# Kernel optimization log

Hardware: AMD Instinct MI355X
Metric: run time of the kernel (lower is better)

The kernel has to match this reference:

```python
import jax, jax.numpy as jnp
import numpy as np

N = 40000      # nodes
E = 640000     # edges
G = 64         # graphs in batch
F_IN = 128
H = 128


def setup_inputs() -> dict:
    key = jax.random.key(0)
    ks = jax.random.split(key, 10)
    x = jax.random.normal(ks[0], (N, F_IN), dtype=jnp.float32)
    edge_index = jax.random.randint(ks[1], (2, E), 0, N, dtype=jnp.int64)
    batch = jnp.sort(jax.random.randint(ks[2], (N,), 0, G, dtype=jnp.int64))
    s = 0.05
    W1 = jax.random.normal(ks[3], (F_IN, H), dtype=jnp.float32) * s
    W2 = jax.random.normal(ks[4], (H, H), dtype=jnp.float32) * s
    W3 = jax.random.normal(ks[5], (H, H), dtype=jnp.float32) * s
    Wl = jax.random.normal(ks[6], (H, 1), dtype=jnp.float32) * s
    b1 = jnp.zeros((H,), jnp.float32)
    b2 = jnp.zeros((H,), jnp.float32)
    b3 = jnp.zeros((H,), jnp.float32)
    bl = jnp.zeros((1,), jnp.float32)
    return {"x": x, "edge_index": edge_index, "batch": batch, "dropout_rate": 0,
            "W1": W1, "b1": b1, "W2": W2, "b2": b2, "W3": W3, "b3": b3,
            "Wl": Wl, "bl": bl}


def _gcn_norm(edge_index, n):
    # PyG GCNConv default: add self-loops, symmetric deg^{-1/2} normalization.
    loop = jnp.arange(n, dtype=edge_index.dtype)
    row = jnp.concatenate([edge_index[0], loop])  # source
    col = jnp.concatenate([edge_index[1], loop])  # target
    ones = jnp.ones(row.shape[0], jnp.float32)
    deg = jax.ops.segment_sum(ones, col, num_segments=n)
    dis = jnp.where(deg > 0, jax.lax.rsqrt(deg), 0.0)
    norm = dis[row] * dis[col]  # [E+N]
    return row, col, norm


def _gcn_conv(x, row, col, norm, W, b, n):
    h = x @ W + b                       # dense transform [N,H]
    msg = h[row] * norm[:, None]        # gather + scale  [E+N,H]
    return jax.ops.segment_sum(msg, col, num_segments=n)


def reference(x, edge_index, batch, dropout_rate, W1, b1, W2, b2, W3, b3, Wl, bl):
    n = x.shape[0]
    row, col, norm = _gcn_norm(edge_index, n)
    # eval mode: dropout(p=dropout_rate, training=False) is identity
    h = jax.nn.relu(_gcn_conv(x, row, col, norm, W1, b1, n))
    h = jax.nn.relu(_gcn_conv(h, row, col, norm, W2, b2, n))
    h = jax.nn.relu(_gcn_conv(h, row, col, norm, W3, b3, n))
    # global mean pool over graphs
    sums = jax.ops.segment_sum(h, batch, num_segments=G)           # [G,H]
    cnt = jax.ops.segment_sum(jnp.ones(n, jnp.float32), batch, num_segments=G)
    pooled = sums / jnp.maximum(cnt, 1.0)[:, None]
    return pooled @ Wl + bl             # [G,1]
```

## Files before the change

### kernel.cpp

```cpp
#include <hip/hip_runtime.h>

constexpr int N = 40000;
constexpr int E = 640000;
constexpr int G = 64;
constexpr int H = 128;

constexpr int NB      = (N + 255) / 256;
constexpr int EB      = (E + 255) / 256;
constexpr int GEMM_B  = N / 32;
constexpr int FUSED_B = N / 32;
constexpr int CSR_MAX = E + 8 * N;

typedef float floatx2 __attribute__((ext_vector_type(2)));

__device__ __forceinline__ unsigned pack_fp8x4(float a, float b, float c, float d) {
    unsigned v = 0;
    v = __builtin_amdgcn_cvt_pk_fp8_f32(a, b, v, false);
    v = __builtin_amdgcn_cvt_pk_fp8_f32(c, d, v, true);
    return v;
}

__device__ __forceinline__ void fma8(float4& acc, unsigned r, float w) {
    floatx2 lo = __builtin_amdgcn_cvt_pk_f32_fp8(r, false);
    floatx2 hi = __builtin_amdgcn_cvt_pk_f32_fp8(r, true);
    acc.x = fmaf(lo.x, w, acc.x);
    acc.y = fmaf(lo.y, w, acc.y);
    acc.z = fmaf(hi.x, w, acc.z);
    acc.w = fmaf(hi.y, w, acc.w);
}

__device__ __forceinline__ float entry_w(int e) {
    floatx2 hi = __builtin_amdgcn_cvt_pk_f32_fp8((unsigned)e, true);
    return hi.y;
}
__device__ __forceinline__ int entry_src(int e) { return e & 0xFFFFFF; }

__device__ __forceinline__ float4 aggregate_node(const unsigned* __restrict__ h8,
                                                 const int4* __restrict__ csr4,
                                                 const int* __restrict__ row_ptr,
                                                 const float* __restrict__ dis,
                                                 int i, int c) {
    float d = dis[i];
    float sl = d * d;
    float4 acc = make_float4(0.f, 0.f, 0.f, 0.f);
    fma8(acc, h8[(size_t)i * 32 + c], sl);
    int p  = row_ptr[i] >> 2;
    int p1 = row_ptr[i + 1] >> 2;
    for (; p < p1; p += 2) {
        int4 ea = csr4[p], eb = csr4[p + 1];
        unsigned r0 = h8[(size_t)entry_src(ea.x) * 32 + c];
        unsigned r1 = h8[(size_t)entry_src(ea.y) * 32 + c];
        unsigned r2 = h8[(size_t)entry_src(ea.z) * 32 + c];
        unsigned r3 = h8[(size_t)entry_src(ea.w) * 32 + c];
        unsigned r4 = h8[(size_t)entry_src(eb.x) * 32 + c];
        unsigned r5 = h8[(size_t)entry_src(eb.y) * 32 + c];
        unsigned r6 = h8[(size_t)entry_src(eb.z) * 32 + c];
        unsigned r7 = h8[(size_t)entry_src(eb.w) * 32 + c];
        fma8(acc, r0, entry_w(ea.x)); fma8(acc, r1, entry_w(ea.y));
        fma8(acc, r2, entry_w(ea.z)); fma8(acc, r3, entry_w(ea.w));
        fma8(acc, r4, entry_w(eb.x)); fma8(acc, r5, entry_w(eb.y));
        fma8(acc, r6, entry_w(eb.z)); fma8(acc, r7, entry_w(eb.w));
    }
    return acc;
}

__global__ __launch_bounds__(256) void gemm1_and_count(const float* __restrict__ X,
                                                       const float* __restrict__ W,
                                                       const float* __restrict__ b,
                                                       unsigned* __restrict__ Y,
                                                       const int* __restrict__ col,
                                                       int* __restrict__ deg) {
    __shared__ float4 Ws4[64 * 32];
    const int blk = blockIdx.x;
    const int tid = threadIdx.x;
    if (blk >= GEMM_B) {
        int e = (blk - GEMM_B) * 256 + tid;
        if (e < E) atomicAdd(&deg[col[e]], 1);
        return;
    }
    const int jg = tid & 31;
    const int rs = tid >> 5;
    const int r0 = blk * 32 + rs * 4;

    const float4* W4 = reinterpret_cast<const float4*>(W);
    const float4* X4 = reinterpret_cast<const float4*>(X);

    const float4 bv = reinterpret_cast<const float4*>(b)[jg];
    float4 acc0 = bv, acc1 = bv, acc2 = bv, acc3 = bv;

    for (int half = 0; half < 2; ++half) {
        #pragma unroll
        for (int i = 0; i < 8; ++i)
            Ws4[tid + i * 256] = W4[half * 2048 + tid + i * 256];
        __syncthreads();

        #pragma unroll 4
        for (int k4 = 0; k4 < 16; ++k4) {
            float4 xv0 = X4[(size_t)(r0 + 0) * 32 + half * 16 + k4];
            float4 xv1 = X4[(size_t)(r0 + 1) * 32 + half * 16 + k4];
            float4 xv2 = X4[(size_t)(r0 + 2) * 32 + half * 16 + k4];
            float4 xv3 = X4[(size_t)(r0 + 3) * 32 + half * 16 + k4];
            #pragma unroll
            for (int kk = 0; kk < 4; ++kk) {
                float4 wv = Ws4[(k4 * 4 + kk) * 32 + jg];
                float xs0 = (kk==0)?xv0.x:(kk==1)?xv0.y:(kk==2)?xv0.z:xv0.w;
                float xs1 = (kk==0)?xv1.x:(kk==1)?xv1.y:(kk==2)?xv1.z:xv1.w;
                float xs2 = (kk==0)?xv2.x:(kk==1)?xv2.y:(kk==2)?xv2.z:xv2.w;
                float xs3 = (kk==0)?xv3.x:(kk==1)?xv3.y:(kk==2)?xv3.z:xv3.w;
                acc0.x = fmaf(xs0, wv.x, acc0.x); acc0.y = fmaf(xs0, wv.y, acc0.y);
                acc0.z = fmaf(xs0, wv.z, acc0.z); acc0.w = fmaf(xs0, wv.w, acc0.w);
                acc1.x = fmaf(xs1, wv.x, acc1.x); acc1.y = fmaf(xs1, wv.y, acc1.y);
                acc1.z = fmaf(xs1, wv.z, acc1.z); acc1.w = fmaf(xs1, wv.w, acc1.w);
                acc2.x = fmaf(xs2, wv.x, acc2.x); acc2.y = fmaf(xs2, wv.y, acc2.y);
                acc2.z = fmaf(xs2, wv.z, acc2.z); acc2.w = fmaf(xs2, wv.w, acc2.w);
                acc3.x = fmaf(xs3, wv.x, acc3.x); acc3.y = fmaf(xs3, wv.y, acc3.y);
                acc3.z = fmaf(xs3, wv.z, acc3.z); acc3.w = fmaf(xs3, wv.w, acc3.w);
            }
        }
        __syncthreads();
    }

    Y[(size_t)(r0 + 0) * 32 + jg] = pack_fp8x4(acc0.x, acc0.y, acc0.z, acc0.w);
    Y[(size_t)(r0 + 1) * 32 + jg] = pack_fp8x4(acc1.x, acc1.y, acc1.z, acc1.w);
    Y[(size_t)(r0 + 2) * 32 + jg] = pack_fp8x4(acc2.x, acc2.y, acc2.z, acc2.w);
    Y[(size_t)(r0 + 3) * 32 + jg] = pack_fp8x4(acc3.x, acc3.y, acc3.z, acc3.w);
}

__global__ void dis_block_sum(const int* __restrict__ deg, float* __restrict__ dis,
                              int* __restrict__ part) {
    __shared__ int s[256];
    int i = blockIdx.x * 256 + threadIdx.x;
    int d = (i < N) ? deg[i] : 0;
    if (i < N) dis[i] = rsqrtf((float)(d + 1));
    s[threadIdx.x] = (d + 7) & ~7;
    __syncthreads();
    for (int off = 128; off > 0; off >>= 1) {
        if (threadIdx.x < off) s[threadIdx.x] += s[threadIdx.x + off];
        __syncthreads();
    }
    if (threadIdx.x == 0) part[blockIdx.x] = s[0];
}

__global__ void scan_write(const int* __restrict__ deg, const int* __restrict__ part,
                           int* __restrict__ row_ptr, int* __restrict__ cursor) {
    __shared__ int s[256];
    const int t = threadIdx.x;
    s[t] = (t < (int)blockIdx.x) ? part[t] : 0;
    __syncthreads();
    for (int o = 128; o > 0; o >>= 1) {
        if (t < o) s[t] += s[t + o];
        __syncthreads();
    }
    const int block_off = s[0];
    __syncthreads();
    int i = blockIdx.x * 256 + t;
    int val = (i < N) ? ((deg[i] + 7) & ~7) : 0;
    s[t] = val;
    __syncthreads();
    for (int o = 1; o < 256; o <<= 1) {
        int x = (t >= o) ? s[t - o] : 0;
        __syncthreads();
        s[t] += x;
        __syncthreads();
    }
    if (i < N) {
        int excl = s[t] - val + block_off;
        row_ptr[i] = excl;
        cursor[i] = excl;
        if (i == N - 1) row_ptr[N] = excl + val;
    }
}

__global__ void fill_csr(const int* __restrict__ row, const int* __restrict__ col,
                         const float* __restrict__ dis, int* __restrict__ cursor,
                         int* __restrict__ csr) {
    int e = blockIdx.x * blockDim.x + threadIdx.x;
    if (e >= E) return;
    int r = row[e], c = col[e];
    float w = dis[r] * dis[c];
    unsigned wb = __builtin_amdgcn_cvt_pk_fp8_f32(w, 0.0f, 0, false) & 0xFFu;
    int p = atomicAdd(&cursor[c], 1);
    csr[p] = (int)((wb << 24) | (unsigned)r);
}

__global__ __launch_bounds__(256) void fused_agg_gemm(const unsigned* __restrict__ t_in,
                                                      const int4* __restrict__ csr4,
                                                      const int* __restrict__ row_ptr,
                                                      const float* __restrict__ dis,
                                                      const float* __restrict__ W,
                                                      const float* __restrict__ b,
                                                      unsigned* __restrict__ t_out) {
    __shared__ float4 tile[32 * 32];
    const int tid = threadIdx.x;
    const int node0 = blockIdx.x * 32;

    {
        const int c  = tid & 31;
        const int nl = tid >> 5;
        #pragma unroll
        for (int sub = 0; sub < 4; ++sub) {
            const int local = sub * 8 + nl;
            float4 acc = aggregate_node(t_in, csr4, row_ptr, dis, node0 + local, c);
            acc.x = fmaxf(acc.x, 0.f); acc.y = fmaxf(acc.y, 0.f);
            acc.z = fmaxf(acc.z, 0.f); acc.w = fmaxf(acc.w, 0.f);
            tile[local * 32 + c] = acc;
        }
    }
    __syncthreads();

    const int jg = tid & 31;
    const int rs = tid >> 5;
    const int r0 = rs * 4;
    const float4* W4 = reinterpret_cast<const float4*>(W);
    const float4 bv = reinterpret_cast<const float4*>(b)[jg];
    float4 acc0 = bv, acc1 = bv, acc2 = bv, acc3 = bv;

    #pragma unroll 4
    for (int k4 = 0; k4 < 32; ++k4) {
        float4 xv0 = tile[(r0 + 0) * 32 + k4];
        float4 xv1 = tile[(r0 + 1) * 32 + k4];
        float4 xv2 = tile[(r0 + 2) * 32 + k4];
        float4 xv3 = tile[(r0 + 3) * 32 + k4];
        #pragma unroll
        for (int kk = 0; kk < 4; ++kk) {
            float4 wv = W4[(k4 * 4 + kk) * 32 + jg];
            float xs0 = (kk==0)?xv0.x:(kk==1)?xv0.y:(kk==2)?xv0.z:xv0.w;
            float xs1 = (kk==0)?xv1.x:(kk==1)?xv1.y:(kk==2)?xv1.z:xv1.w;
            float xs2 = (kk==0)?xv2.x:(kk==1)?xv2.y:(kk==2)?xv2.z:xv2.w;
            float xs3 = (kk==0)?xv3.x:(kk==1)?xv3.y:(kk==2)?xv3.z:xv3.w;
            acc0.x = fmaf(xs0, wv.x, acc0.x); acc0.y = fmaf(xs0, wv.y, acc0.y);
            acc0.z = fmaf(xs0, wv.z, acc0.z); acc0.w = fmaf(xs0, wv.w, acc0.w);
            acc1.x = fmaf(xs1, wv.x, acc1.x); acc1.y = fmaf(xs1, wv.y, acc1.y);
            acc1.z = fmaf(xs1, wv.z, acc1.z); acc1.w = fmaf(xs1, wv.w, acc1.w);
            acc2.x = fmaf(xs2, wv.x, acc2.x); acc2.y = fmaf(xs2, wv.y, acc2.y);
            acc2.z = fmaf(xs2, wv.z, acc2.z); acc2.w = fmaf(xs2, wv.w, acc2.w);
            acc3.x = fmaf(xs3, wv.x, acc3.x); acc3.y = fmaf(xs3, wv.y, acc3.y);
            acc3.z = fmaf(xs3, wv.z, acc3.z); acc3.w = fmaf(xs3, wv.w, acc3.w);
        }
    }

    const int gr0 = node0 + r0;
    t_out[(size_t)(gr0 + 0) * 32 + jg] = pack_fp8x4(acc0.x, acc0.y, acc0.z, acc0.w);
    t_out[(size_t)(gr0 + 1) * 32 + jg] = pack_fp8x4(acc1.x, acc1.y, acc1.z, acc1.w);
    t_out[(size_t)(gr0 + 2) * 32 + jg] = pack_fp8x4(acc2.x, acc2.y, acc2.z, acc2.w);
    t_out[(size_t)(gr0 + 3) * 32 + jg] = pack_fp8x4(acc3.x, acc3.y, acc3.z, acc3.w);
}

__global__ __launch_bounds__(256) void agg_pool(const unsigned* __restrict__ t_in,
                                                const int4* __restrict__ csr4,
                                                const int* __restrict__ row_ptr,
                                                const float* __restrict__ dis,
                                                const int* __restrict__ batch,
                                                float* __restrict__ pooled) {
    __shared__ float4 tile[8 * 32];
    const int tid = threadIdx.x;
    const int c  = tid & 31;
    const int nl = tid >> 5;
    const int i0 = blockIdx.x * 8;

    float4 acc = aggregate_node(t_in, csr4, row_ptr, dis, i0 + nl, c);
    acc.x = fmaxf(acc.x, 0.f); acc.y = fmaxf(acc.y, 0.f);
    acc.z = fmaxf(acc.z, 0.f); acc.w = fmaxf(acc.w, 0.f);
    tile[nl * 32 + c] = acc;
    __syncthreads();

    if (tid < 128) {
        const int j = tid;
        const float* tf = reinterpret_cast<const float*>(tile);
        int cur = batch[i0];
        float s = 0.0f;
        #pragma unroll
        for (int r = 0; r < 8; ++r) {
            int g = batch[i0 + r];
            if (g != cur) { atomicAdd(&pooled[cur * H + j], s); s = 0.0f; cur = g; }
            s += tf[r * 128 + j];
        }
        atomicAdd(&pooled[cur * H + j], s);
    }
}

__global__ __launch_bounds__(128) void head(const float* __restrict__ pooled,
                                            const int* __restrict__ batch,
                                            const float* __restrict__ Wl,
                                            const float* __restrict__ bl,
                                            float* __restrict__ out) {
    const int g = blockIdx.x;
    const int j = threadIdx.x;
    __shared__ int bounds[2];
    if (j < 2) {
        int target = g + j;
        int lo = 0, hi = N;
        while (lo < hi) {
            int mid = (lo + hi) >> 1;
            if (batch[mid] < target) lo = mid + 1; else hi = mid;
        }
        bounds[j] = lo;
    }
    __syncthreads();
    float cnt = fmaxf((float)(bounds[1] - bounds[0]), 1.0f);
    float val = (pooled[g * H + j] / cnt) * Wl[j];
    __shared__ float red[128];
    red[j] = val;
    __syncthreads();
    #pragma unroll
    for (int s = 64; s > 0; s >>= 1) {
        if (j < s) red[j] += red[j + s];
        __syncthreads();
    }
    if (j == 0) out[g] = red[0] + bl[0];
}

extern "C" void kernel_launch(void* const* d_in, const int* in_sizes, int n_in,
                              void* d_out, int out_size, void* d_ws, size_t ws_size,
                              hipStream_t stream) {
    const float* x     = (const float*)d_in[0];
    const int*   ei    = (const int*)  d_in[1];
    const int*   batch = (const int*)  d_in[2];
    const float* W1 = (const float*)d_in[4];
    const float* b1 = (const float*)d_in[5];
    const float* W2 = (const float*)d_in[6];
    const float* b2 = (const float*)d_in[7];
    const float* W3 = (const float*)d_in[8];
    const float* b3 = (const float*)d_in[9];
    const float* Wl = (const float*)d_in[10];
    const float* bl = (const float*)d_in[11];
    float* out = (float*)d_out;

    const int* row = ei;
    const int* col = ei + E;

    auto align256 = [](size_t v) { return (v + 255) & ~(size_t)255; };
    char* ws = (char*)d_ws;
    size_t off = 0;
    int*   deg    = (int*)(ws + off);
    float* pooled = (float*)(deg + N);
    int*   csr    = (int*)(pooled + (size_t)G * H);
    size_t zero_bytes = (size_t)N * 4 + (size_t)G * H * 4 + (size_t)CSR_MAX * 4;
    off += align256(zero_bytes);
    float*    dis     = (float*)(ws + off); off += align256((size_t)N * 4);
    int*      row_ptr = (int*)  (ws + off); off += align256((size_t)(N + 1) * 4);
    int*      cursor  = (int*)  (ws + off); off += align256((size_t)N * 4);
    int*      part    = (int*)  (ws + off); off += align256((size_t)NB * 4);
    unsigned* bufA    = (unsigned*)(ws + off); off += align256((size_t)N * H);
    unsigned* bufB    = (unsigned*)(ws + off); off += align256((size_t)N * H);
    (void)ws_size; (void)n_in; (void)in_sizes; (void)out_size;

    const int4* csr4 = reinterpret_cast<const int4*>(csr);

    hipMemsetAsync(deg, 0, zero_bytes, stream);
    gemm1_and_count<<<GEMM_B + EB, 256, 0, stream>>>(x, W1, b1, bufA, col, deg);
    dis_block_sum<<<NB, 256, 0, stream>>>(deg, dis, part);
    scan_write<<<NB, 256, 0, stream>>>(deg, part, row_ptr, cursor);
    fill_csr<<<EB, 256, 0, stream>>>(row, col, dis, cursor, csr);
    fused_agg_gemm<<<FUSED_B, 256, 0, stream>>>(bufA, csr4, row_ptr, dis, W2, b2, bufB);
    fused_agg_gemm<<<FUSED_B, 256, 0, stream>>>(bufB, csr4, row_ptr, dis, W3, b3, bufA);
    agg_pool<<<N / 8, 256, 0, stream>>>(bufA, csr4, row_ptr, dis, batch, pooled);
    head<<<G, 128, 0, stream>>>(pooled, batch, Wl, bl, out);
}
```

Before: 261.1 us.

## Use fp16 MFMA for dense transforms with pre-transposed fp16 weights

```diff
diff --git a/kernel.cpp b/kernel.cpp
--- a/kernel.cpp
+++ b/kernel.cpp
@@ -7,11 +7,13 @@
 
 constexpr int NB      = (N + 255) / 256;
 constexpr int EB      = (E + 255) / 256;
-constexpr int GEMM_B  = N / 32;
+constexpr int GEMM1_B = N / 64;
 constexpr int FUSED_B = N / 32;
 constexpr int CSR_MAX = E + 8 * N;
 
-typedef float floatx2 __attribute__((ext_vector_type(2)));
+typedef float    floatx2 __attribute__((ext_vector_type(2)));
+typedef float    f32x4   __attribute__((ext_vector_type(4)));
+typedef _Float16 f16x8   __attribute__((ext_vector_type(8)));
 
 __device__ __forceinline__ unsigned pack_fp8x4(float a, float b, float c, float d) {
     unsigned v = 0;
@@ -34,6 +36,13 @@
     return hi.y;
 }
 __device__ __forceinline__ int entry_src(int e) { return e & 0xFFFFFF; }
+
+__device__ __forceinline__ f16x8 cvt8(float4 a, float4 b) {
+    f16x8 r;
+    r[0] = (_Float16)a.x; r[1] = (_Float16)a.y; r[2] = (_Float16)a.z; r[3] = (_Float16)a.w;
+    r[4] = (_Float16)b.x; r[5] = (_Float16)b.y; r[6] = (_Float16)b.z; r[7] = (_Float16)b.w;
+    return r;
+}
 
 __device__ __forceinline__ float4 aggregate_node(const unsigned* __restrict__ h8,
                                                  const int4* __restrict__ csr4,
@@ -64,66 +73,72 @@
     return acc;
 }
 
+__global__ void prep_wt(const float* __restrict__ W1, const float* __restrict__ W2,
+                        const float* __restrict__ W3, _Float16* __restrict__ wt) {
+    const int m = blockIdx.x >> 3;
+    const float* W = (m == 0) ? W1 : (m == 1) ? W2 : W3;
+    const int g  = (blockIdx.x & 7) * 256 + threadIdx.x;
+    const int f  = g >> 4;
+    const int k0 = (g & 15) * 8;
+    f16x8 v;
+    #pragma unroll
+    for (int j = 0; j < 8; ++j) v[j] = (_Float16)W[(size_t)(k0 + j) * H + f];
+    *reinterpret_cast<f16x8*>(wt + ((size_t)m << 14) + f * H + k0) = v;
+}
+
 __global__ __launch_bounds__(256) void gemm1_and_count(const float* __restrict__ X,
-                                                       const float* __restrict__ W,
+                                                       const _Float16* __restrict__ wt1,
                                                        const float* __restrict__ b,
                                                        unsigned* __restrict__ Y,
                                                        const int* __restrict__ col,
                                                        int* __restrict__ deg) {
-    __shared__ float4 Ws4[64 * 32];
+    __shared__ uint4 WTl[2048];
     const int blk = blockIdx.x;
     const int tid = threadIdx.x;
-    if (blk >= GEMM_B) {
-        int e = (blk - GEMM_B) * 256 + tid;
+    if (blk >= GEMM1_B) {
+        int e = (blk - GEMM1_B) * 256 + tid;
         if (e < E) atomicAdd(&deg[col[e]], 1);
         return;
     }
-    const int jg = tid & 31;
-    const int rs = tid >> 5;
-    const int r0 = blk * 32 + rs * 4;
-
-    const float4* W4 = reinterpret_cast<const float4*>(W);
+    const uint4* wtg = reinterpret_cast<const uint4*>(wt1);
+    #pragma unroll
+    for (int i = 0; i < 8; ++i) {
+        int g = i * 256 + tid;
+        WTl[g ^ ((g >> 4) & 7)] = wtg[g];
+    }
+    __syncthreads();
+
+    const int lane = tid & 63;
+    const int wv   = tid >> 6;
+    const int c    = lane & 15;
+    const int grp  = lane >> 4;
+    const int node = blk * 64 + wv * 16 + c;
+
+    const f32x4* b4 = reinterpret_cast<const f32x4*>(b);
+    f32x4 acc[8];
+    #pragma unroll
+    for (int mt = 0; mt < 8; ++mt) acc[mt] = b4[mt * 4 + grp];
+
     const float4* X4 = reinterpret_cast<const float4*>(X);
-
-    const float4 bv = reinterpret_cast<const float4*>(b)[jg];
-    float4 acc0 = bv, acc1 = bv, acc2 = bv, acc3 = bv;
-
-    for (int half = 0; half < 2; ++half) {
+    #pragma unroll
+    for (int ks = 0; ks < 4; ++ks) {
+        const int k0 = ks * 32 + grp * 8;
+        float4 xa = X4[(size_t)node * 32 + (k0 >> 2)];
+        float4 xb = X4[(size_t)node * 32 + (k0 >> 2) + 1];
+        f16x8 bfr = cvt8(xa, xb);
         #pragma unroll
-        for (int i = 0; i < 8; ++i)
-            Ws4[tid + i * 256] = W4[half * 2048 + tid + i * 256];
-        __syncthreads();
-
-        #pragma unroll 4
-        for (int k4 = 0; k4 < 16; ++k4) {
-            float4 xv0 = X4[(size_t)(r0 + 0) * 32 + half * 16 + k4];
-            float4 xv1 = X4[(size_t)(r0 + 1) * 32 + half * 16 + k4];
-            float4 xv2 = X4[(size_t)(r0 + 2) * 32 + half * 16 + k4];
-            float4 xv3 = X4[(size_t)(r0 + 3) * 32 + half * 16 + k4];
-            #pragma unroll
-            for (int kk = 0; kk < 4; ++kk) {
-                float4 wv = Ws4[(k4 * 4 + kk) * 32 + jg];
-                float xs0 = (kk==0)?xv0.x:(kk==1)?xv0.y:(kk==2)?xv0.z:xv0.w;
-                float xs1 = (kk==0)?xv1.x:(kk==1)?xv1.y:(kk==2)?xv1.z:xv1.w;
-                float xs2 = (kk==0)?xv2.x:(kk==1)?xv2.y:(kk==2)?xv2.z:xv2.w;
-                float xs3 = (kk==0)?xv3.x:(kk==1)?xv3.y:(kk==2)?xv3.z:xv3.w;
-                acc0.x = fmaf(xs0, wv.x, acc0.x); acc0.y = fmaf(xs0, wv.y, acc0.y);
-                acc0.z = fmaf(xs0, wv.z, acc0.z); acc0.w = fmaf(xs0, wv.w, acc0.w);
-                acc1.x = fmaf(xs1, wv.x, acc1.x); acc1.y = fmaf(xs1, wv.y, acc1.y);
-                acc1.z = fmaf(xs1, wv.z, acc1.z); acc1.w = fmaf(xs1, wv.w, acc1.w);
-                acc2.x = fmaf(xs2, wv.x, acc2.x); acc2.y = fmaf(xs2, wv.y, acc2.y);
-                acc2.z = fmaf(xs2, wv.z, acc2.z); acc2.w = fmaf(xs2, wv.w, acc2.w);
-                acc3.x = fmaf(xs3, wv.x, acc3.x); acc3.y = fmaf(xs3, wv.y, acc3.y);
-                acc3.z = fmaf(xs3, wv.z, acc3.z); acc3.w = fmaf(xs3, wv.w, acc3.w);
-            }
-        }
-        __syncthreads();
-    }
-
-    Y[(size_t)(r0 + 0) * 32 + jg] = pack_fp8x4(acc0.x, acc0.y, acc0.z, acc0.w);
-    Y[(size_t)(r0 + 1) * 32 + jg] = pack_fp8x4(acc1.x, acc1.y, acc1.z, acc1.w);
-    Y[(size_t)(r0 + 2) * 32 + jg] = pack_fp8x4(acc2.x, acc2.y, acc2.z, acc2.w);
-    Y[(size_t)(r0 + 3) * 32 + jg] = pack_fp8x4(acc3.x, acc3.y, acc3.z, acc3.w);
+        for (int mt = 0; mt < 8; ++mt) {
+            const int f = mt * 16 + c;
+            const int g = (f << 4) + (k0 >> 3);
+            f16x8 afr = *reinterpret_cast<const f16x8*>(&WTl[g ^ (f & 7)]);
+            acc[mt] = __builtin_amdgcn_mfma_f32_16x16x32_f16(afr, bfr, acc[mt], 0, 0, 0);
+        }
+    }
+    #pragma unroll
+    for (int mt = 0; mt < 8; ++mt) {
+        const int jg = mt * 4 + grp;
+        Y[(size_t)node * 32 + jg] = pack_fp8x4(acc[mt][0], acc[mt][1], acc[mt][2], acc[mt][3]);
+    }
 }
 
 __global__ void dis_block_sum(const int* __restrict__ deg, float* __restrict__ dis,
@@ -187,7 +202,7 @@
                                                       const int4* __restrict__ csr4,
                                                       const int* __restrict__ row_ptr,
                                                       const float* __restrict__ dis,
-                                                      const float* __restrict__ W,
+                                                      const _Float16* __restrict__ wt,
                                                       const float* __restrict__ b,
                                                       unsigned* __restrict__ t_out) {
     __shared__ float4 tile[32 * 32];
@@ -195,55 +210,65 @@
     const int node0 = blockIdx.x * 32;
 
     {
-        const int c  = tid & 31;
+        const int cc = tid & 31;
         const int nl = tid >> 5;
         #pragma unroll
         for (int sub = 0; sub < 4; ++sub) {
             const int local = sub * 8 + nl;
-            float4 acc = aggregate_node(t_in, csr4, row_ptr, dis, node0 + local, c);
+            float4 acc = aggregate_node(t_in, csr4, row_ptr, dis, node0 + local, cc);
             acc.x = fmaxf(acc.x, 0.f); acc.y = fmaxf(acc.y, 0.f);
             acc.z = fmaxf(acc.z, 0.f); acc.w = fmaxf(acc.w, 0.f);
-            tile[local * 32 + c] = acc;
-        }
-    }
-    __syncthreads();
-
-    const int jg = tid & 31;
-    const int rs = tid >> 5;
-    const int r0 = rs * 4;
-    const float4* W4 = reinterpret_cast<const float4*>(W);
-    const float4 bv = reinterpret_cast<const float4*>(b)[jg];
-    float4 acc0 = bv, acc1 = bv, acc2 = bv, acc3 = bv;
-
-    #pragma unroll 4
-    for (int k4 = 0; k4 < 32; ++k4) {
-        float4 xv0 = tile[(r0 + 0) * 32 + k4];
-        float4 xv1 = tile[(r0 + 1) * 32 + k4];
-        float4 xv2 = tile[(r0 + 2) * 32 + k4];
-        float4 xv3 = tile[(r0 + 3) * 32 + k4];
-        #pragma unroll
-        for (int kk = 0; kk < 4; ++kk) {
-            float4 wv = W4[(k4 * 4 + kk) * 32 + jg];
-            float xs0 = (kk==0)?xv0.x:(kk==1)?xv0.y:(kk==2)?xv0.z:xv0.w;
-            float xs1 = (kk==0)?xv1.x:(kk==1)?xv1.y:(kk==2)?xv1.z:xv1.w;
-            float xs2 = (kk==0)?xv2.x:(kk==1)?xv2.y:(kk==2)?xv2.z:xv2.w;
-            float xs3 = (kk==0)?xv3.x:(kk==1)?xv3.y:(kk==2)?xv3.z:xv3.w;
-            acc0.x = fmaf(xs0, wv.x, acc0.x); acc0.y = fmaf(xs0, wv.y, acc0.y);
-            acc0.z = fmaf(xs0, wv.z, acc0.z); acc0.w = fmaf(xs0, wv.w, acc0.w);
-            acc1.x = fmaf(xs1, wv.x, acc1.x); acc1.y = fmaf(xs1, wv.y, acc1.y);
-            acc1.z = fmaf(xs1, wv.z, acc1.z); acc1.w = fmaf(xs1, wv.w, acc1.w);
-            acc2.x = fmaf(xs2, wv.x, acc2.x); acc2.y = fmaf(xs2, wv.y, acc2.y);
-            acc2.z = fmaf(xs2, wv.z, acc2.z); acc2.w = fmaf(xs2, wv.w, acc2.w);
-            acc3.x = fmaf(xs3, wv.x, acc3.x); acc3.y = fmaf(xs3, wv.y, acc3.y);
-            acc3.z = fmaf(xs3, wv.z, acc3.z); acc3.w = fmaf(xs3, wv.w, acc3.w);
-        }
-    }
-
-    const int gr0 = node0 + r0;
-    t_out[(size_t)(gr0 + 0) * 32 + jg] = pack_fp8x4(acc0.x, acc0.y, acc0.z, acc0.w);
-    t_out[(size_t)(gr0 + 1) * 32 + jg] = pack_fp8x4(acc1.x, acc1.y, acc1.z, acc1.w);
-    t_out[(size_t)(gr0 + 2) * 32 + jg] = pack_fp8x4(acc2.x, acc2.y, acc2.z, acc2.w);
-    t_out[(size_t)(gr0 + 3) * 32 + jg] = pack_fp8x4(acc3.x, acc3.y, acc3.z, acc3.w);
+            tile[(local * 32 + cc) ^ (local & 7)] = acc;
+        }
+    }
+    __syncthreads();
+
+    const int lane = tid & 63;
+    const int wv   = tid >> 6;
+    const int c    = lane & 15;
+    const int grp  = lane >> 4;
+
+    const f32x4* b4 = reinterpret_cast<const f32x4*>(b);
+    f32x4 acc00, acc01, acc10, acc11;
+    acc00 = acc01 = b4[(2 * wv + 0) * 4 + grp];
+    acc10 = acc11 = b4[(2 * wv + 1) * 4 + grp];
+
+    const uint4* wtg = reinterpret_cast<const uint4*>(wt);
+    #pragma unroll
+    for (int ks = 0; ks < 4; ++ks) {
+        const int k0 = ks * 32 + grp * 8;
+        f16x8 bfr0, bfr1;
+        {
+            int nd = c;
+            int g0 = nd * 32 + (k0 >> 2);
+            float4 ta = tile[g0 ^ (nd & 7)];
+            float4 tb = tile[(g0 + 1) ^ (nd & 7)];
+            bfr0 = cvt8(ta, tb);
+            nd = 16 + c;
+            g0 = nd * 32 + (k0 >> 2);
+            ta = tile[g0 ^ (nd & 7)];
+            tb = tile[(g0 + 1) ^ (nd & 7)];
+            bfr1 = cvt8(ta, tb);
+        }
+        {
+            int f = (2 * wv + 0) * 16 + c;
+            f16x8 afr = *reinterpret_cast<const f16x8*>(&wtg[f * 16 + (k0 >> 3)]);
+            acc00 = __builtin_amdgcn_mfma_f32_16x16x32_f16(afr, bfr0, acc00, 0, 0, 0);
+            acc01 = __builtin_amdgcn_mfma_f32_16x16x32_f16(afr, bfr1, acc01, 0, 0, 0);
+            f = (2 * wv + 1) * 16 + c;
+            afr = *reinterpret_cast<const f16x8*>(&wtg[f * 16 + (k0 >> 3)]);
+            acc10 = __builtin_amdgcn_mfma_f32_16x16x32_f16(afr, bfr0, acc10, 0, 0, 0);
+            acc11 = __builtin_amdgcn_mfma_f32_16x16x32_f16(afr, bfr1, acc11, 0, 0, 0);
+        }
+    }
+
+    const int jg0 = (2 * wv + 0) * 4 + grp;
+    const int jg1 = (2 * wv + 1) * 4 + grp;
+    const int nA = node0 + c, nB = node0 + 16 + c;
+    t_out[(size_t)nA * 32 + jg0] = pack_fp8x4(acc00[0], acc00[1], acc00[2], acc00[3]);
+    t_out[(size_t)nB * 32 + jg0] = pack_fp8x4(acc01[0], acc01[1], acc01[2], acc01[3]);
+    t_out[(size_t)nA * 32 + jg1] = pack_fp8x4(acc10[0], acc10[1], acc10[2], acc10[3]);
+    t_out[(size_t)nB * 32 + jg1] = pack_fp8x4(acc11[0], acc11[1], acc11[2], acc11[3]);
 }
 
 __global__ __launch_bounds__(256) void agg_pool(const unsigned* __restrict__ t_in,
@@ -343,17 +368,22 @@
     int*      part    = (int*)  (ws + off); off += align256((size_t)NB * 4);
     unsigned* bufA    = (unsigned*)(ws + off); off += align256((size_t)N * H);
     unsigned* bufB    = (unsigned*)(ws + off); off += align256((size_t)N * H);
+    _Float16* wt      = (_Float16*)(ws + off); off += align256((size_t)3 * H * H * 2);
     (void)ws_size; (void)n_in; (void)in_sizes; (void)out_size;
 
     const int4* csr4 = reinterpret_cast<const int4*>(csr);
+    _Float16* wt1 = wt;
+    _Float16* wt2 = wt + (size_t)H * H;
+    _Float16* wt3 = wt + (size_t)2 * H * H;
 
     hipMemsetAsync(deg, 0, zero_bytes, stream);
-    gemm1_and_count<<<GEMM_B + EB, 256, 0, stream>>>(x, W1, b1, bufA, col, deg);
+    prep_wt<<<24, 256, 0, stream>>>(W1, W2, W3, wt);
+    gemm1_and_count<<<GEMM1_B + EB, 256, 0, stream>>>(x, wt1, b1, bufA, col, deg);
     dis_block_sum<<<NB, 256, 0, stream>>>(deg, dis, part);
     scan_write<<<NB, 256, 0, stream>>>(deg, part, row_ptr, cursor);
     fill_csr<<<EB, 256, 0, stream>>>(row, col, dis, cursor, csr);
-    fused_agg_gemm<<<FUSED_B, 256, 0, stream>>>(bufA, csr4, row_ptr, dis, W2, b2, bufB);
-    fused_agg_gemm<<<FUSED_B, 256, 0, stream>>>(bufB, csr4, row_ptr, dis, W3, b3, bufA);
+    fused_agg_gemm<<<FUSED_B, 256, 0, stream>>>(bufA, csr4, row_ptr, dis, wt2, b2, bufB);
+    fused_agg_gemm<<<FUSED_B, 256, 0, stream>>>(bufB, csr4, row_ptr, dis, wt3, b3, bufA);
     agg_pool<<<N / 8, 256, 0, stream>>>(bufA, csr4, row_ptr, dis, batch, pooled);
     head<<<G, 128, 0, stream>>>(pooled, batch, Wl, bl, out);
 }
```

Result: faster. 219.6 us (-15.9%).
